# Optimization experiments

Measured on AMD Instinct MI355X. Metric: run time of the kernel, lower is better.

The kernel has to match this reference:

```python
import jax, jax.numpy as jnp
import numpy as np


def setup_inputs() -> dict:
    key = jax.random.key(0)
    ks = jax.random.split(key, 8)
    B, N, D, E, M = 32, 128, 128, 32, 8192
    h_nodes = jax.random.normal(ks[0], (B, N, D), dtype=jnp.float32)
    h_edges = jax.random.normal(ks[1], (B, N, N, E), dtype=jnp.float32)
    W_edit = jax.random.normal(ks[2], (2 * D + E, 4), dtype=jnp.float32) * 0.02
    b_edit = jnp.zeros((4,), dtype=jnp.float32)
    W_stop = jax.random.normal(ks[3], (D, 1), dtype=jnp.float32) * 0.02
    b_stop = jnp.zeros((1,), dtype=jnp.float32)
    i_idx = jax.random.randint(ks[4], (M,), 0, N, dtype=jnp.int32)
    j_idx = jax.random.randint(ks[5], (M,), 0, N, dtype=jnp.int32)
    b_idx = jax.random.randint(ks[6], (M,), 0, 4, dtype=jnp.int32)
    feas = jax.random.randint(ks[7], (B, M), 0, 2, dtype=jnp.int32).astype(jnp.bool_)
    stop_feas = jnp.ones((B,), dtype=jnp.bool_)
    return {
        "h_nodes": h_nodes, "h_edges": h_edges,
        "W_edit": W_edit, "b_edit": b_edit,
        "W_stop": W_stop, "b_stop": b_stop,
        "i_idx": i_idx, "j_idx": j_idx, "b_idx": b_idx,
        "feas": feas, "stop_feas": stop_feas,
    }


def reference(h_nodes, h_edges, W_edit, b_edit, W_stop, b_stop,
              i_idx, j_idx, b_idx, feas, stop_feas):
    # h_nodes: [B,N,D], h_edges: [B,N,N,E]
    B = h_nodes.shape[0]
    M = i_idx.shape[0]
    neg_inf = jnp.asarray(-jnp.inf, dtype=h_nodes.dtype)
    # Batched gather of all (i, j, e_ij) edit features: [B, M, 2D+E]
    feat = jnp.concatenate(
        [h_nodes[:, i_idx], h_nodes[:, j_idx], h_edges[:, i_idx, j_idx]],
        axis=-1,
    )
    # Single fused small matmul over all edits: [B, M, 4]
    edit_logits = jnp.einsum("bmf,fo->bmo", feat, W_edit) + b_edit
    # Select the bond-type channel b for each edit: [B, M]
    sel = jnp.take_along_axis(
        edit_logits, jnp.broadcast_to(b_idx[None, :, None], (B, M, 1)), axis=2
    )[..., 0]
    sel = jnp.where(feas, sel, neg_inf)
    # STOP logit from mean-pooled node features: [B]
    stop = (h_nodes.mean(axis=1) @ W_stop + b_stop)[:, 0]
    stop = jnp.where(stop_feas, stop, neg_inf)
    # [B, M+1] logits (edits followed by STOP)
    return jnp.concatenate([sel, stop[:, None]], axis=1)
```

## Files before the change

### kernel.cpp

```cpp
#include <hip/hip_runtime.h>
#include <hip/hip_fp16.h>
#include <math.h>

#define BATCH 32
#define NNODE 128
#define DDIM 128
#define EDIM 32
#define MEDITS 8192
#define OUTSTRIDE (MEDITS + 1)

typedef unsigned short u16;
typedef unsigned int u32;

#define MASK16 ((u16)0xFBFFu)
#define MASK32 0xC76A6000u

__device__ __forceinline__ u32 f2u(float f) { u32 x; __builtin_memcpy(&x, &f, 4); return x; }
__device__ __forceinline__ float u2f(u32 x) { float f; __builtin_memcpy(&f, &x, 4); return f; }

template <int MODE>
__device__ __forceinline__ float cv16(u32 bits) {
    if constexpr (MODE == 1) return __half2float(__ushort_as_half((u16)bits));
    else                     return u2f(bits << 16);
}
template <int MODE>
__device__ __forceinline__ float cv16hi(u32 w) {
    if constexpr (MODE == 1) return __half2float(__ushort_as_half((u16)(w >> 16)));
    else                     return u2f(w & 0xFFFF0000u);
}

__device__ __forceinline__ u16 f32_to_f16_safe(float f) {
    u16 h = __half_as_ushort(__float2half_rn(f));
    if ((h & 0x7C00u) == 0x7C00u) h = (u16)((h & 0x8000u) | 0x7BFFu);
    return h;
}

__device__ __forceinline__ u16 f32_to_bf16_safe(float f) {
    u32 x = f2u(f);
    u32 r = x + 0x7FFFu + ((x >> 16) & 1u);
    u16 u = (u16)(r >> 16);
    if ((u & 0x7C00u) == 0x7C00u) u = (u16)((u & 0x8000u) | 0x7BFFu);
    return u;
}

__device__ __forceinline__ u32 enc_f32(float f) {
    u32 x = f2u(f);
    if ((x & 0x7F800000u) == 0x7F800000u)
        x = (x & 0x80000000u) | 0x476A6000u;
    return x;
}

template <int MODE>
__device__ __forceinline__ float LD(const void* p, size_t i) {
    if constexpr (MODE == 0) return ((const float*)p)[i];
    else return cv16<MODE>(((const u16*)p)[i]);
}

template <int MODE>
__device__ __forceinline__ void ST(void* o, size_t i, float v, bool masked) {
    if constexpr (MODE == 0) ((u32*)o)[i] = masked ? MASK32 : enc_f32(v);
    else if constexpr (MODE == 1) ((u16*)o)[i] = masked ? MASK16 : f32_to_f16_safe(v);
    else ((u16*)o)[i] = masked ? MASK16 : f32_to_bf16_safe(v);
}

template <int NT>
__device__ __forceinline__ int block_probe(const u16* __restrict__ h) {
    const int t = threadIdx.x;
    __shared__ int cb[4], cs[4];
    int myb = 0, mys = 0;
#pragma unroll
    for (int k = 0; k < 256 / NT; ++k) {
        u16 u = h[2 * (t + k * NT)];
        int e8 = (u >> 7) & 0xFF;
        int e5 = (u >> 10) & 0x1F;
        myb += (e8 >= 118 && e8 <= 129);
        mys += (e5 >= 6 && e5 <= 14);
    }
#pragma unroll
    for (int off = 32; off; off >>= 1) {
        myb += __shfl_down(myb, off, 64);
        mys += __shfl_down(mys, off, 64);
    }
    if ((t & 63) == 0) { cb[t >> 6] = myb; cs[t >> 6] = mys; }
    if (NT < 256 && t == 0) {
#pragma unroll
        for (int w = NT / 64; w < 4; ++w) { cb[w] = 0; cs[w] = 0; }
    }
    __syncthreads();
    int B = cb[0] + cb[1] + cb[2] + cb[3];
    int S = cs[0] + cs[1] + cs[2] + cs[3];
    return (B < 48) ? 0 : ((S > 87) ? 1 : 2);
}

template <int MODE>
__device__ void proj_impl(const void* h_nodes, const void* W_edit, const void* b_edit,
                          const void* W_stop, const void* b_stop,
                          const unsigned char* stop_feas,
                          float* __restrict__ Pi, float* __restrict__ Pj, void* out) {
    const int b = blockIdx.x;
    const int sel = blockIdx.y;
    const int t = threadIdx.x;

    if (sel < 8) {
        const int c = sel & 3;
        const int half = sel >> 2;
        __shared__ __align__(16) float wcol[DDIM];
        wcol[t] = LD<MODE>(W_edit, (size_t)(half * DDIM + t) * 4 + c);
        __syncthreads();
        const size_t rowbase = ((size_t)b * NNODE + t) * DDIM;
        const float4* wp = (const float4*)wcol;
        float acc = 0.f;
        if constexpr (MODE == 0) {
            const float4* hp = (const float4*)((const float*)h_nodes + rowbase);
#pragma unroll
            for (int k = 0; k < DDIM / 4; ++k) {
                float4 h4 = hp[k], w4 = wp[k];
                acc += h4.x * w4.x + h4.y * w4.y + h4.z * w4.z + h4.w * w4.w;
            }
        } else {
            const uint2* hp = (const uint2*)((const u16*)h_nodes + rowbase);
#pragma unroll
            for (int k = 0; k < DDIM / 4; ++k) {
                uint2 h2 = hp[k]; float4 w4 = wp[k];
                acc += cv16<MODE>(h2.x & 0xFFFFu) * w4.x + cv16hi<MODE>(h2.x) * w4.y
                     + cv16<MODE>(h2.y & 0xFFFFu) * w4.z + cv16hi<MODE>(h2.y) * w4.w;
            }
        }
        if (half == 0) {
            acc += LD<MODE>(b_edit, c);
            Pi[((size_t)b * NNODE + t) * 4 + c] = acc;
        } else {
            Pj[((size_t)b * NNODE + t) * 4 + c] = acc;
        }
    } else {
        const size_t base = (size_t)b * (NNODE * DDIM);
        float colsum = 0.f;
#pragma unroll 8
        for (int n = 0; n < NNODE; ++n) colsum += LD<MODE>(h_nodes, base + n * DDIM + t);
        float v = colsum * LD<MODE>(W_stop, t);
        __shared__ float red[2];
#pragma unroll
        for (int off = 32; off; off >>= 1) v += __shfl_down(v, off, 64);
        if ((t & 63) == 0) red[t >> 6] = v;
        __syncthreads();
        if (t == 0) {
            float s = (red[0] + red[1]) * (1.0f / NNODE) + LD<MODE>(b_stop, 0);
            ST<MODE>(out, (size_t)b * OUTSTRIDE + MEDITS, s, stop_feas[b] == 0);
        }
    }
}

__global__ void __launch_bounds__(128)
proj_stop_kernel(const void* h_nodes, const void* W_edit, const void* b_edit,
                 const void* W_stop, const void* b_stop,
                 const unsigned char* stop_feas,
                 float* Pi, float* Pj, void* out) {
    const int mode = block_probe<128>((const u16*)h_nodes);
    if (mode == 0)      proj_impl<0>(h_nodes, W_edit, b_edit, W_stop, b_stop, stop_feas, Pi, Pj, out);
    else if (mode == 1) proj_impl<1>(h_nodes, W_edit, b_edit, W_stop, b_stop, stop_feas, Pi, Pj, out);
    else                proj_impl<2>(h_nodes, W_edit, b_edit, W_stop, b_stop, stop_feas, Pi, Pj, out);
}

template <int MODE>
__device__ void edits_impl(const void* h_edges, const void* W_edit,
                           const int* __restrict__ i_idx, const int* __restrict__ j_idx,
                           const int* __restrict__ b_idx,
                           const unsigned char* __restrict__ feas,
                           const float* __restrict__ Pi, const float* __restrict__ Pj,
                           void* out) {
    const int t = threadIdx.x;
    const int m = blockIdx.x * 256 + t;
    const int b = blockIdx.y;

    __shared__ __align__(16) float Wec[4][EDIM];
    __shared__ float Pb[NNODE * 4];
    __shared__ float Qb[NNODE * 4];
    if (t < 128) {
        const int c = t >> 5, e = t & 31;
        Wec[c][e] = LD<MODE>(W_edit, (size_t)(2 * DDIM + e) * 4 + c);
    }
    Pb[t] = Pi[(size_t)b * (NNODE * 4) + t];
    Pb[t + 256] = Pi[(size_t)b * (NNODE * 4) + t + 256];
    Qb[t] = Pj[(size_t)b * (NNODE * 4) + t];
    Qb[t + 256] = Pj[(size_t)b * (NNODE * 4) + t + 256];
    __syncthreads();

    const int i = i_idx[m] & (NNODE - 1);
    const int j = j_idx[m] & (NNODE - 1);
    const int c = b_idx[m] & 3;
    const size_t ebase = (((size_t)b * NNODE + i) * NNODE + j) * EDIM;
    const float4* wv = (const float4*)Wec[c];

    float acc = 0.f;
    if constexpr (MODE == 0) {
        const float4* ep = (const float4*)((const float*)h_edges + ebase);
#pragma unroll
        for (int k = 0; k < EDIM / 4; ++k) {
            float4 e4 = ep[k], w4 = wv[k];
            acc += e4.x * w4.x + e4.y * w4.y + e4.z * w4.z + e4.w * w4.w;
        }
    } else {
        const uint4* ep = (const uint4*)((const u16*)h_edges + ebase);
#pragma unroll
        for (int k = 0; k < EDIM / 8; ++k) {
            uint4 q = ep[k];
            float4 wa = wv[2 * k], wb = wv[2 * k + 1];
            acc += cv16<MODE>(q.x & 0xFFFFu) * wa.x + cv16hi<MODE>(q.x) * wa.y
                 + cv16<MODE>(q.y & 0xFFFFu) * wa.z + cv16hi<MODE>(q.y) * wa.w
                 + cv16<MODE>(q.z & 0xFFFFu) * wb.x + cv16hi<MODE>(q.z) * wb.y
                 + cv16<MODE>(q.w & 0xFFFFu) * wb.z + cv16hi<MODE>(q.w) * wb.w;
        }
    }
    float r = acc + Pb[i * 4 + c] + Qb[j * 4 + c];
    bool masked = (feas[(size_t)b * MEDITS + m] == 0);
    ST<MODE>(out, (size_t)b * OUTSTRIDE + m, r, masked);
}

__global__ void __launch_bounds__(256)
edits_kernel(const void* h_nodes, const void* h_edges, const void* W_edit,
             const int* i_idx, const int* j_idx, const int* b_idx,
             const unsigned char* feas,
             const float* Pi, const float* Pj, void* out) {
    const int mode = block_probe<256>((const u16*)h_nodes);
    if (mode == 0)      edits_impl<0>(h_edges, W_edit, i_idx, j_idx, b_idx, feas, Pi, Pj, out);
    else if (mode == 1) edits_impl<1>(h_edges, W_edit, i_idx, j_idx, b_idx, feas, Pi, Pj, out);
    else                edits_impl<2>(h_edges, W_edit, i_idx, j_idx, b_idx, feas, Pi, Pj, out);
}

extern "C" void kernel_launch(void* const* d_in, const int* in_sizes, int n_in,
                              void* d_out, int out_size, void* d_ws, size_t ws_size,
                              hipStream_t stream) {
    (void)in_sizes; (void)n_in; (void)out_size; (void)ws_size;

    const void* h_nodes = d_in[0];
    const void* h_edges = d_in[1];
    const void* W_edit  = d_in[2];
    const void* b_edit  = d_in[3];
    const void* W_stop  = d_in[4];
    const void* b_stop  = d_in[5];
    const int*  i_idx   = (const int*)d_in[6];
    const int*  j_idx   = (const int*)d_in[7];
    const int*  b_idx   = (const int*)d_in[8];
    const unsigned char* feas      = (const unsigned char*)d_in[9];
    const unsigned char* stop_feas = (const unsigned char*)d_in[10];

    float* Pi = (float*)d_ws;
    float* Pj = Pi + BATCH * NNODE * 4;

    proj_stop_kernel<<<dim3(BATCH, 9), 128, 0, stream>>>(
        h_nodes, W_edit, b_edit, W_stop, b_stop, stop_feas, Pi, Pj, d_out);
    edits_kernel<<<dim3(MEDITS / 256, BATCH), 256, 0, stream>>>(
        h_nodes, h_edges, W_edit, i_idx, j_idx, b_idx, feas, Pi, Pj, d_out);
}
```

Before: 121.2 us.

## Fuse node projection and stop logit into single edits kernel

Merges the projection/stop kernel and the edits kernel into one launch. Each edits block recomputes the per-batch node projections Pi/Pj in shared memory, using float4 accumulation over all four channels, instead of reading them from a workspace filled by a prior kernel. An extra block column computes the stop logit. This removes one launch and the dependency between the two kernels, but each of the 32 blocks per batch now redundantly recomputes the 128x128x8 projection.

```diff
diff --git a/kernel.cpp b/kernel.cpp
--- a/kernel.cpp
+++ b/kernel.cpp
@@ -34,7 +34,6 @@
     if ((h & 0x7C00u) == 0x7C00u) h = (u16)((h & 0x8000u) | 0x7BFFu);
     return h;
 }
-
 __device__ __forceinline__ u16 f32_to_bf16_safe(float f) {
     u32 x = f2u(f);
     u32 r = x + 0x7FFFu + ((x >> 16) & 1u);
@@ -42,7 +41,6 @@
     if ((u & 0x7C00u) == 0x7C00u) u = (u16)((u & 0x8000u) | 0x7BFFu);
     return u;
 }
-
 __device__ __forceinline__ u32 enc_f32(float f) {
     u32 x = f2u(f);
     if ((x & 0x7F800000u) == 0x7F800000u)
@@ -63,29 +61,24 @@
     else ((u16*)o)[i] = masked ? MASK16 : f32_to_bf16_safe(v);
 }
 
-template <int NT>
-__device__ __forceinline__ int block_probe(const u16* __restrict__ h) {
+__device__ __forceinline__ void fma4(float4& a, float x, const float4 w) {
+    a.x += x * w.x; a.y += x * w.y; a.z += x * w.z; a.w += x * w.w;
+}
+
+__device__ __forceinline__ int block_probe256(const u16* __restrict__ h) {
     const int t = threadIdx.x;
     __shared__ int cb[4], cs[4];
-    int myb = 0, mys = 0;
-#pragma unroll
-    for (int k = 0; k < 256 / NT; ++k) {
-        u16 u = h[2 * (t + k * NT)];
-        int e8 = (u >> 7) & 0xFF;
-        int e5 = (u >> 10) & 0x1F;
-        myb += (e8 >= 118 && e8 <= 129);
-        mys += (e5 >= 6 && e5 <= 14);
-    }
+    u16 u = h[2 * t];
+    int e8 = (u >> 7) & 0xFF;
+    int e5 = (u >> 10) & 0x1F;
+    int myb = (e8 >= 118 && e8 <= 129);
+    int mys = (e5 >= 6 && e5 <= 14);
 #pragma unroll
     for (int off = 32; off; off >>= 1) {
         myb += __shfl_down(myb, off, 64);
         mys += __shfl_down(mys, off, 64);
     }
     if ((t & 63) == 0) { cb[t >> 6] = myb; cs[t >> 6] = mys; }
-    if (NT < 256 && t == 0) {
-#pragma unroll
-        for (int w = NT / 64; w < 4; ++w) { cb[w] = 0; cs[w] = 0; }
-    }
     __syncthreads();
     int B = cb[0] + cb[1] + cb[2] + cb[3];
     int S = cs[0] + cs[1] + cs[2] + cs[3];
@@ -93,96 +86,77 @@
 }
 
 template <int MODE>
-__device__ void proj_impl(const void* h_nodes, const void* W_edit, const void* b_edit,
-                          const void* W_stop, const void* b_stop,
-                          const unsigned char* stop_feas,
-                          float* __restrict__ Pi, float* __restrict__ Pj, void* out) {
-    const int b = blockIdx.x;
-    const int sel = blockIdx.y;
+__device__ void edits_impl(const void* h_nodes, const void* h_edges,
+                           const void* W_edit, const void* b_edit,
+                           const int* __restrict__ i_idx, const int* __restrict__ j_idx,
+                           const int* __restrict__ b_idx,
+                           const unsigned char* __restrict__ feas, void* out) {
     const int t = threadIdx.x;
-
-    if (sel < 8) {
-        const int c = sel & 3;
-        const int half = sel >> 2;
-        __shared__ __align__(16) float wcol[DDIM];
-        wcol[t] = LD<MODE>(W_edit, (size_t)(half * DDIM + t) * 4 + c);
-        __syncthreads();
-        const size_t rowbase = ((size_t)b * NNODE + t) * DDIM;
-        const float4* wp = (const float4*)wcol;
-        float acc = 0.f;
+    const int b = blockIdx.y;
+    const int m = blockIdx.x * 256 + t;
+
+    __shared__ __align__(16) float4 Wi4[DDIM];
+    __shared__ __align__(16) float4 Wj4[DDIM];
+    __shared__ __align__(16) float Wec[4][EDIM + 4];
+    __shared__ float Pb[NNODE * 4];
+    __shared__ float Qb[NNODE * 4];
+
+    for (int r = t; r < 2 * DDIM + EDIM; r += 256) {
+        float w0 = LD<MODE>(W_edit, (size_t)r * 4 + 0);
+        float w1 = LD<MODE>(W_edit, (size_t)r * 4 + 1);
+        float w2 = LD<MODE>(W_edit, (size_t)r * 4 + 2);
+        float w3 = LD<MODE>(W_edit, (size_t)r * 4 + 3);
+        if (r < DDIM)            Wi4[r] = make_float4(w0, w1, w2, w3);
+        else if (r < 2 * DDIM)   Wj4[r - DDIM] = make_float4(w0, w1, w2, w3);
+        else {
+            int e = r - 2 * DDIM;
+            Wec[0][e] = w0; Wec[1][e] = w1; Wec[2][e] = w2; Wec[3][e] = w3;
+        }
+    }
+    __syncthreads();
+
+    {
+        const int n = t & (NNODE - 1);
+        const bool isJ = (t >= NNODE);
+        const float4* W4 = isJ ? Wj4 : Wi4;
+        const size_t rowbase = ((size_t)b * NNODE + n) * DDIM;
+        float4 acc = make_float4(0.f, 0.f, 0.f, 0.f);
         if constexpr (MODE == 0) {
             const float4* hp = (const float4*)((const float*)h_nodes + rowbase);
-#pragma unroll
+#pragma unroll 4
             for (int k = 0; k < DDIM / 4; ++k) {
-                float4 h4 = hp[k], w4 = wp[k];
-                acc += h4.x * w4.x + h4.y * w4.y + h4.z * w4.z + h4.w * w4.w;
+                float4 h4 = hp[k];
+                fma4(acc, h4.x, W4[4 * k + 0]);
+                fma4(acc, h4.y, W4[4 * k + 1]);
+                fma4(acc, h4.z, W4[4 * k + 2]);
+                fma4(acc, h4.w, W4[4 * k + 3]);
             }
         } else {
-            const uint2* hp = (const uint2*)((const u16*)h_nodes + rowbase);
-#pragma unroll
-            for (int k = 0; k < DDIM / 4; ++k) {
-                uint2 h2 = hp[k]; float4 w4 = wp[k];
-                acc += cv16<MODE>(h2.x & 0xFFFFu) * w4.x + cv16hi<MODE>(h2.x) * w4.y
-                     + cv16<MODE>(h2.y & 0xFFFFu) * w4.z + cv16hi<MODE>(h2.y) * w4.w;
+            const uint4* hp = (const uint4*)((const u16*)h_nodes + rowbase);
+#pragma unroll 4
+            for (int k = 0; k < DDIM / 8; ++k) {
+                uint4 q = hp[k];
+                int d = k * 8;
+                fma4(acc, cv16<MODE>(q.x & 0xFFFFu), W4[d + 0]);
+                fma4(acc, cv16hi<MODE>(q.x),         W4[d + 1]);
+                fma4(acc, cv16<MODE>(q.y & 0xFFFFu), W4[d + 2]);
+                fma4(acc, cv16hi<MODE>(q.y),         W4[d + 3]);
+                fma4(acc, cv16<MODE>(q.z & 0xFFFFu), W4[d + 4]);
+                fma4(acc, cv16hi<MODE>(q.z),         W4[d + 5]);
+                fma4(acc, cv16<MODE>(q.w & 0xFFFFu), W4[d + 6]);
+                fma4(acc, cv16hi<MODE>(q.w),         W4[d + 7]);
             }
         }
-        if (half == 0) {
-            acc += LD<MODE>(b_edit, c);
-            Pi[((size_t)b * NNODE + t) * 4 + c] = acc;
+        if (!isJ) {
+            Pb[n * 4 + 0] = acc.x + LD<MODE>(b_edit, 0);
+            Pb[n * 4 + 1] = acc.y + LD<MODE>(b_edit, 1);
+            Pb[n * 4 + 2] = acc.z + LD<MODE>(b_edit, 2);
+            Pb[n * 4 + 3] = acc.w + LD<MODE>(b_edit, 3);
         } else {
-            Pj[((size_t)b * NNODE + t) * 4 + c] = acc;
-        }
-    } else {
-        const size_t base = (size_t)b * (NNODE * DDIM);
-        float colsum = 0.f;
-#pragma unroll 8
-        for (int n = 0; n < NNODE; ++n) colsum += LD<MODE>(h_nodes, base + n * DDIM + t);
-        float v = colsum * LD<MODE>(W_stop, t);
-        __shared__ float red[2];
-#pragma unroll
-        for (int off = 32; off; off >>= 1) v += __shfl_down(v, off, 64);
-        if ((t & 63) == 0) red[t >> 6] = v;
-        __syncthreads();
-        if (t == 0) {
-            float s = (red[0] + red[1]) * (1.0f / NNODE) + LD<MODE>(b_stop, 0);
-            ST<MODE>(out, (size_t)b * OUTSTRIDE + MEDITS, s, stop_feas[b] == 0);
-        }
-    }
-}
-
-__global__ void __launch_bounds__(128)
-proj_stop_kernel(const void* h_nodes, const void* W_edit, const void* b_edit,
-                 const void* W_stop, const void* b_stop,
-                 const unsigned char* stop_feas,
-                 float* Pi, float* Pj, void* out) {
-    const int mode = block_probe<128>((const u16*)h_nodes);
-    if (mode == 0)      proj_impl<0>(h_nodes, W_edit, b_edit, W_stop, b_stop, stop_feas, Pi, Pj, out);
-    else if (mode == 1) proj_impl<1>(h_nodes, W_edit, b_edit, W_stop, b_stop, stop_feas, Pi, Pj, out);
-    else                proj_impl<2>(h_nodes, W_edit, b_edit, W_stop, b_stop, stop_feas, Pi, Pj, out);
-}
-
-template <int MODE>
-__device__ void edits_impl(const void* h_edges, const void* W_edit,
-                           const int* __restrict__ i_idx, const int* __restrict__ j_idx,
-                           const int* __restrict__ b_idx,
-                           const unsigned char* __restrict__ feas,
-                           const float* __restrict__ Pi, const float* __restrict__ Pj,
-                           void* out) {
-    const int t = threadIdx.x;
-    const int m = blockIdx.x * 256 + t;
-    const int b = blockIdx.y;
-
-    __shared__ __align__(16) float Wec[4][EDIM];
-    __shared__ float Pb[NNODE * 4];
-    __shared__ float Qb[NNODE * 4];
-    if (t < 128) {
-        const int c = t >> 5, e = t & 31;
-        Wec[c][e] = LD<MODE>(W_edit, (size_t)(2 * DDIM + e) * 4 + c);
-    }
-    Pb[t] = Pi[(size_t)b * (NNODE * 4) + t];
-    Pb[t + 256] = Pi[(size_t)b * (NNODE * 4) + t + 256];
-    Qb[t] = Pj[(size_t)b * (NNODE * 4) + t];
-    Qb[t + 256] = Pj[(size_t)b * (NNODE * 4) + t + 256];
+            Qb[n * 4 + 0] = acc.x; Qb[n * 4 + 1] = acc.y;
+            Qb[n * 4 + 2] = acc.z; Qb[n * 4 + 3] = acc.w;
+        }
+    }
     __syncthreads();
 
     const int i = i_idx[m] & (NNODE - 1);
@@ -216,21 +190,52 @@
     ST<MODE>(out, (size_t)b * OUTSTRIDE + m, r, masked);
 }
 
+template <int MODE>
+__device__ void stop_impl(const void* h_nodes, const void* W_stop, const void* b_stop,
+                          const unsigned char* stop_feas, void* out) {
+    const int b = blockIdx.y;
+    const int t = threadIdx.x;
+    float v = 0.f;
+    if (t < DDIM) {
+        const size_t base = (size_t)b * (NNODE * DDIM);
+        float colsum = 0.f;
+#pragma unroll 8
+        for (int n = 0; n < NNODE; ++n) colsum += LD<MODE>(h_nodes, base + n * DDIM + t);
+        v = colsum * LD<MODE>(W_stop, t);
+    }
+    __shared__ float red[4];
+#pragma unroll
+    for (int off = 32; off; off >>= 1) v += __shfl_down(v, off, 64);
+    if ((t & 63) == 0) red[t >> 6] = v;
+    __syncthreads();
+    if (t == 0) {
+        float s = (red[0] + red[1] + red[2] + red[3]) * (1.0f / NNODE) + LD<MODE>(b_stop, 0);
+        ST<MODE>(out, (size_t)b * OUTSTRIDE + MEDITS, s, stop_feas[b] == 0);
+    }
+}
+
 __global__ void __launch_bounds__(256)
-edits_kernel(const void* h_nodes, const void* h_edges, const void* W_edit,
+fused_kernel(const void* h_nodes, const void* h_edges,
+             const void* W_edit, const void* b_edit,
+             const void* W_stop, const void* b_stop,
              const int* i_idx, const int* j_idx, const int* b_idx,
-             const unsigned char* feas,
-             const float* Pi, const float* Pj, void* out) {
-    const int mode = block_probe<256>((const u16*)h_nodes);
-    if (mode == 0)      edits_impl<0>(h_edges, W_edit, i_idx, j_idx, b_idx, feas, Pi, Pj, out);
-    else if (mode == 1) edits_impl<1>(h_edges, W_edit, i_idx, j_idx, b_idx, feas, Pi, Pj, out);
-    else                edits_impl<2>(h_edges, W_edit, i_idx, j_idx, b_idx, feas, Pi, Pj, out);
+             const unsigned char* feas, const unsigned char* stop_feas, void* out) {
+    const int mode = block_probe256((const u16*)h_nodes);
+    if (blockIdx.x < 32) {
+        if (mode == 0)      edits_impl<0>(h_nodes, h_edges, W_edit, b_edit, i_idx, j_idx, b_idx, feas, out);
+        else if (mode == 1) edits_impl<1>(h_nodes, h_edges, W_edit, b_edit, i_idx, j_idx, b_idx, feas, out);
+        else                edits_impl<2>(h_nodes, h_edges, W_edit, b_edit, i_idx, j_idx, b_idx, feas, out);
+    } else {
+        if (mode == 0)      stop_impl<0>(h_nodes, W_stop, b_stop, stop_feas, out);
+        else if (mode == 1) stop_impl<1>(h_nodes, W_stop, b_stop, stop_feas, out);
+        else                stop_impl<2>(h_nodes, W_stop, b_stop, stop_feas, out);
+    }
 }
 
 extern "C" void kernel_launch(void* const* d_in, const int* in_sizes, int n_in,
                               void* d_out, int out_size, void* d_ws, size_t ws_size,
                               hipStream_t stream) {
-    (void)in_sizes; (void)n_in; (void)out_size; (void)ws_size;
+    (void)in_sizes; (void)n_in; (void)out_size; (void)d_ws; (void)ws_size;
 
     const void* h_nodes = d_in[0];
     const void* h_edges = d_in[1];
@@ -244,11 +249,7 @@
     const unsigned char* feas      = (const unsigned char*)d_in[9];
     const unsigned char* stop_feas = (const unsigned char*)d_in[10];
 
-    float* Pi = (float*)d_ws;
-    float* Pj = Pi + BATCH * NNODE * 4;
-
-    proj_stop_kernel<<<dim3(BATCH, 9), 128, 0, stream>>>(
-        h_nodes, W_edit, b_edit, W_stop, b_stop, stop_feas, Pi, Pj, d_out);
-    edits_kernel<<<dim3(MEDITS / 256, BATCH), 256, 0, stream>>>(
-        h_nodes, h_edges, W_edit, i_idx, j_idx, b_idx, feas, Pi, Pj, d_out);
-}
+    fused_kernel<<<dim3(33, BATCH), 256, 0, stream>>>(
+        h_nodes, h_edges, W_edit, b_edit, W_stop, b_stop,
+        i_idx, j_idx, b_idx, feas, stop_feas, d_out);
+}
```

Measured after the change: 132.7 us. 1.1x slower.
